# Performance work log

Measured on AMD Instinct MI355X. Metric: run time of the kernel, lower is better.

## Reference

```python
import jax, jax.numpy as jnp
import numpy as np

SCALE = 2      # shuffle_scale
K = 3          # nearest neighbors / conv kernel size (stride == K)
SAMPLES = 16   # sample grid size per axis -> M = SAMPLES**2


def pixel_unshuffle(x, s):
    B, C, H, W = x.shape
    x = x.reshape(B, C, H // s, s, W // s, s)
    x = x.transpose(0, 1, 3, 5, 2, 4)
    return x.reshape(B, C * s * s, H // s, W // s)


def pixel_shuffle(x, s):
    B, C, H, W = x.shape
    x = x.reshape(B, C // (s * s), s, s, H, W)
    x = x.transpose(0, 1, 4, 2, 5, 3)
    return x.reshape(B, C // (s * s), H * s, W * s)


def setup_inputs() -> dict:
    key = jax.random.key(0)
    k1, k2, k3 = jax.random.split(key, 3)
    x = jax.random.normal(k1, (32, 16, 128, 128), dtype=jnp.float32)
    weight = jax.random.normal(k2, (64, 64, K), dtype=jnp.float32) * 0.05  # [out_1d, in_1d, K]
    bias = jax.random.normal(k3, (64,), dtype=jnp.float32) * 0.05
    return {"x": x, "weight": weight, "bias": bias}


def reference(x, weight, bias):
    # --- pixel unshuffle ('B' part of 'BA') ---
    x1 = pixel_unshuffle(x, SCALE)                 # [B, C1=64, H1=64, W1=64]
    B, C1, H1, W1 = x1.shape
    N = H1 * W1

    # --- spatial subsample grid (linspace + round, sample_padding=0) ---
    xi = jnp.round(jnp.linspace(0.0, H1 - 1.0, SAMPLES)).astype(jnp.int32)
    yi = jnp.round(jnp.linspace(0.0, W1 - 1.0, SAMPLES)).astype(jnp.int32)
    xg, yg = jnp.meshgrid(xi, yi, indexing="ij")
    x_sample = x1[:, :, xg, yg].reshape(B, C1, -1)  # [B, C1, M]
    x2 = x1.reshape(B, C1, N)                       # [B, C1, N]

    # --- pairwise squared euclidean distance tokens -> samples ---
    # (sqrt omitted: monotone; top-k uses only indices, matching torch topk(largest=False))
    n2 = jnp.sum(x2 * x2, axis=1)                   # [B, N]
    m2 = jnp.sum(x_sample * x_sample, axis=1)       # [B, M]
    dot = jnp.einsum("bcn,bcm->bnm", x2, x_sample)  # [B, N, M]
    d2 = n2[:, :, None] + m2[:, None, :] - 2.0 * dot

    # --- K nearest sampled points per token ---
    _, idx = jax.lax.top_k(-d2, K)                  # [B, N, K]

    # --- gather neighbor features ('prime'); equals x2 at flat_indices[idx] ---
    prime = jnp.take_along_axis(x_sample[:, :, None, :], idx[:, None, :, :], axis=3)  # [B, C1, N, K]

    # --- Conv1d(kernel=K, stride=K) over [B, C1, N*K] == per-token contraction ---
    out = jnp.einsum("bcnk,ock->bon", prime, weight) + bias[None, :, None]  # [B, O1=64, N]
    out = out.reshape(B, weight.shape[0], H1, W1)

    # --- pixel shuffle ('A' part of 'BA') ---
    return pixel_shuffle(out, SCALE)                # [B, 16, 128, 128]
```

## Files before the change

kernel.cpp:

```cpp
#include <hip/hip_runtime.h>
#include <cstdint>
#include <cfloat>

typedef float v2f __attribute__((ext_vector_type(2)));

__constant__ int c_smp[16] = {0,4,8,13,17,21,25,29,34,38,42,46,50,55,59,63};

static constexpr int NB   = 32;
static constexpr int NC   = 64;
static constexpr int NH   = 64;
static constexpr int NTOK = 4096;
static constexpr int NM   = 256;
static constexpr int NK   = 3;

__global__ __launch_bounds__(256) void k_pre(const float* __restrict__ x,
                                             const float* __restrict__ w,
                                             float* __restrict__ wT,
                                             float* __restrict__ xs_t) {
    __shared__ __align__(16) float rows[16][2][128];
    if (blockIdx.x >= NB * 16) {
        int f = (blockIdx.x - NB * 16) * 256 + threadIdx.x;
        float v = w[f];
        int o = f / 192, rem = f % 192;
        int c = rem / 3, k = rem % 3;
        wT[((size_t)k * 64 + c) * 64 + o] = v;
        return;
    }
    int b = blockIdx.x >> 4, gi = blockIdx.x & 15;
    int hh = c_smp[gi];
    int t = threadIdx.x;
    const float* xb = x + (size_t)b * 16 * 128 * 128;
#pragma unroll
    for (int it = 0; it < 4; ++it) {
        int q = t + it * 256;
        int c = q >> 6;
        int rem = q & 63;
        int sh = rem >> 5;
        int col = (rem & 31) * 4;
        float4 v = *(const float4*)(xb + ((size_t)c * 128 + (2 * hh + sh)) * 128 + col);
        *(float4*)&rows[c][sh][col] = v;
    }
    __syncthreads();
    {
        int c1 = t >> 2;
        int c = c1 >> 2, sh = (c1 >> 1) & 1, sw = c1 & 1;
        int gj0 = (t & 3) * 4;
        float4 v;
        v.x = rows[c][sh][2 * c_smp[gj0 + 0] + sw];
        v.y = rows[c][sh][2 * c_smp[gj0 + 1] + sw];
        v.z = rows[c][sh][2 * c_smp[gj0 + 2] + sw];
        v.w = rows[c][sh][2 * c_smp[gj0 + 3] + sw];
        *(float4*)&xs_t[((size_t)b * NC + c1) * NM + gi * 16 + gj0] = v;
    }
}

__global__ __launch_bounds__(256) void k_z2(const float* __restrict__ xs_t,
                                            const float* __restrict__ wT,
                                            float* __restrict__ Z) {
    __shared__ __align__(16) float wL[64][64];
    __shared__ __align__(16) float xt[16][64];
    int bid = blockIdx.x;
    int mq = bid & 3;
    int k  = (bid >> 2) % 3;
    int b  = bid / 12;
    int t  = threadIdx.x;
    int mg = t >> 4, og = t & 15;

#pragma unroll
    for (int it = 0; it < 4; ++it) {
        int q = t + it * 256;
        int c = q >> 4;
        int o4 = (q & 15) * 4;
        *(float4*)&wL[c][o4] = *(const float4*)&wT[(size_t)k * 4096 + q * 4];
    }

    v2f acc[4][2];
#pragma unroll
    for (int i = 0; i < 4; ++i) { acc[i][0] = (v2f)(0.f); acc[i][1] = (v2f)(0.f); }

    for (int cc = 0; cc < 4; ++cc) {
        __syncthreads();
        {
            int c = t >> 4, m4 = (t & 15) * 4;
            *(float4*)&xt[c][m4] =
                *(const float4*)&xs_t[((size_t)b * NC + cc * 16 + c) * NM + mq * 64 + m4];
        }
        __syncthreads();
#pragma unroll
        for (int c = 0; c < 16; ++c) {
            float4 a4 = *(const float4*)&xt[c][mg * 4];
            float4 b4 = *(const float4*)&wL[cc * 16 + c][og * 4];
            v2f bp0 = {b4.x, b4.y}, bp1 = {b4.z, b4.w};
            float aa[4] = {a4.x, a4.y, a4.z, a4.w};
#pragma unroll
            for (int i = 0; i < 4; ++i) {
                v2f ai = {aa[i], aa[i]};
                acc[i][0] = __builtin_elementwise_fma(ai, bp0, acc[i][0]);
                acc[i][1] = __builtin_elementwise_fma(ai, bp1, acc[i][1]);
            }
        }
    }

    float* zb = Z + (((size_t)b * 3 + k) * NM + mq * 64) * NC;
#pragma unroll
    for (int i = 0; i < 4; ++i) {
        int m = mg * 4 + i;
        float4 v = {acc[i][0][0], acc[i][0][1], acc[i][1][0], acc[i][1][1]};
        *(float4*)&zb[(size_t)m * NC + og * 4] = v;
    }
}

static __device__ __forceinline__ unsigned long long packkey(float d, int m) {
    unsigned u = __float_as_uint(d);
    u ^= ((unsigned)((int)u >> 31)) | 0x80000000u;
    return ((unsigned long long)u << 32) | (unsigned)m;
}

__global__ __launch_bounds__(256) void k_do(const float* __restrict__ x,
                                            const float* __restrict__ xs_t,
                                            const float* __restrict__ Z,
                                            const float* __restrict__ bias,
                                            float* __restrict__ out) {
    __shared__ __align__(16) float smem[5632];
    float (*att)[64]  = (float(*)[64])smem;
    float (*xsB)[256] = (float(*)[256])(smem + 1024);
    float* m2l = smem + 5120;
    float* n2l = smem + 5376;
    int  (*idxL)[3] = (int(*)[3])(smem + 5440);
    float* staged = smem;

    int b = blockIdx.x >> 6;
    int h = blockIdx.x & 63;
    int t = threadIdx.x;
    int r = t >> 4, cl = t & 15;

    v2f acc2[4][8];
#pragma unroll
    for (int i = 0; i < 4; ++i)
#pragma unroll
        for (int j = 0; j < 8; ++j) acc2[i][j] = (v2f)(0.f);

    float m2acc = 0.f, n2acc = 0.f;
    const float* xb = x + (size_t)b * 16 * 128 * 128;
    const float* xsb = xs_t + (size_t)b * NC * NM;

    for (int kc = 0; kc < 4; ++kc) {
        __syncthreads();
#pragma unroll
        for (int it = 0; it < 2; ++it) {
            int i = t + it * 256;
            int p = i >> 6;
            int wcol = i & 63;
            int c1e = kc * 16 + p * 2;
            int c = c1e >> 2, sh = (c1e >> 1) & 1;
            const float* src = xb + ((size_t)c * 128 + (2 * h + sh)) * 128 + 2 * wcol;
            float2 v = *(const float2*)src;
            att[p * 2 + 0][wcol] = v.x;
            att[p * 2 + 1][wcol] = v.y;
        }
#pragma unroll
        for (int it = 0; it < 4; ++it) {
            int g = t + it * 256;
            int row = g >> 6;
            int m4 = g & 63;
            int dst = ((((m4 & 3) << 4) | (m4 >> 2))) << 2;
            *(float4*)&xsB[row][dst] =
                *(const float4*)&xsb[(size_t)(kc * 16 + row) * NM + m4 * 4];
        }
        __syncthreads();

#pragma unroll
        for (int c = 0; c < 16; ++c) {
            float v = xsB[c][t];
            m2acc = __fadd_rn(m2acc, __fmul_rn(v, v));
        }
        if (t < 64) {
#pragma unroll
            for (int c = 0; c < 16; ++c) {
                float v = att[c][t];
                n2acc = __fadd_rn(n2acc, __fmul_rn(v, v));
            }
        }

#pragma unroll
        for (int k = 0; k < 16; ++k) {
            float4 a0 = *(const float4*)&att[k][r * 4];
            float4 b0 = *(const float4*)&xsB[k][(0 * 16 + cl) * 4];
            float4 b1 = *(const float4*)&xsB[k][(1 * 16 + cl) * 4];
            float4 b2 = *(const float4*)&xsB[k][(2 * 16 + cl) * 4];
            float4 b3 = *(const float4*)&xsB[k][(3 * 16 + cl) * 4];
            v2f bp0 = {b0.x, b0.y}, bp1 = {b0.z, b0.w};
            v2f bp2 = {b1.x, b1.y}, bp3 = {b1.z, b1.w};
            v2f bp4 = {b2.x, b2.y}, bp5 = {b2.z, b2.w};
            v2f bp6 = {b3.x, b3.y}, bp7 = {b3.z, b3.w};
            float aa[4] = {a0.x, a0.y, a0.z, a0.w};
#pragma unroll
            for (int i = 0; i < 4; ++i) {
                v2f ai = {aa[i], aa[i]};
                acc2[i][0] = __builtin_elementwise_fma(ai, bp0, acc2[i][0]);
                acc2[i][1] = __builtin_elementwise_fma(ai, bp1, acc2[i][1]);
                acc2[i][2] = __builtin_elementwise_fma(ai, bp2, acc2[i][2]);
                acc2[i][3] = __builtin_elementwise_fma(ai, bp3, acc2[i][3]);
                acc2[i][4] = __builtin_elementwise_fma(ai, bp4, acc2[i][4]);
                acc2[i][5] = __builtin_elementwise_fma(ai, bp5, acc2[i][5]);
                acc2[i][6] = __builtin_elementwise_fma(ai, bp6, acc2[i][6]);
                acc2[i][7] = __builtin_elementwise_fma(ai, bp7, acc2[i][7]);
            }
        }
    }

    m2l[((t >> 2) & 15) * 16 + (t >> 6) * 4 + (t & 3)] = m2acc;
    if (t < 64) n2l[t] = n2acc;
    __syncthreads();

    float m2r[16];
#pragma unroll
    for (int j = 0; j < 16; ++j) m2r[j] = m2l[cl * 16 + j];

#pragma unroll
    for (int i = 0; i < 4; ++i) {
        int nloc = r * 4 + i;
        float n2v = n2l[nloc];
        float e0d = FLT_MAX, e1d = FLT_MAX, e2d = FLT_MAX;
        int e0m = 0x7fffffff, e1m = 0x7fffffff, e2m = 0x7fffffff;
#pragma unroll
        for (int j = 0; j < 16; ++j) {
            float dv = acc2[i][j >> 1][j & 1];
            float t1 = __fadd_rn(n2v, m2r[j]);
            float d = __fadd_rn(t1, -2.0f * dv);
            int m = cl * 16 + j;
            if (d < e2d) {
                e2d = d; e2m = m;
                if (e2d < e1d) {
                    float td = e1d; int tm = e1m; e1d = e2d; e1m = e2m;
                    e2d = td; e2m = tm;
                    if (e1d < e0d) {
                        float sd = e0d; int sm = e0m; e0d = e1d; e0m = e1m;
                        e1d = sd; e1m = sm;
                    }
                }
            }
        }
        unsigned long long k0 = packkey(e0d, e0m);
        unsigned long long k1 = packkey(e1d, e1m);
        unsigned long long k2 = packkey(e2d, e2m);
#pragma unroll
        for (int mask = 1; mask <= 8; mask <<= 1) {
            unsigned long long q0 = __shfl_xor(k0, mask);
            unsigned long long q1 = __shfl_xor(k1, mask);
            unsigned long long q2 = __shfl_xor(k2, mask);
            unsigned long long clo = k0 < q0 ? k0 : q0;
            unsigned long long chi = k0 < q0 ? q0 : k0;
            unsigned long long dlo = k1 < q1 ? k1 : q1;
            unsigned long long dhi = k1 < q1 ? q1 : k1;
            unsigned long long f2  = k2 < q2 ? k2 : q2;
            unsigned long long elo = chi < dlo ? chi : dlo;
            unsigned long long ehi = chi < dlo ? dlo : chi;
            unsigned long long g2  = dhi < f2 ? dhi : f2;
            k0 = clo;
            k1 = elo;
            k2 = ehi < g2 ? ehi : g2;
        }
        if (cl == 0) {
            idxL[nloc][0] = (int)(unsigned)(k0 & 0xffffffffu);
            idxL[nloc][1] = (int)(unsigned)(k1 & 0xffffffffu);
            idxL[nloc][2] = (int)(unsigned)(k2 & 0xffffffffu);
        }
    }
    __syncthreads();

    {
        int o = t & 63, wv = t >> 6;
        float bv = bias[o];
        const float* zb = Z + (size_t)b * 3 * NM * NC;
        for (int ti = 0; ti < 16; ++ti) {
            int w = wv * 16 + ti;
            int i0 = idxL[w][0], i1 = idxL[w][1], i2 = idxL[w][2];
            float v = bv + zb[(size_t)i0 * NC + o]
                         + zb[(size_t)(NM + i1) * NC + o]
                         + zb[(size_t)(2 * NM + i2) * NC + o];
            staged[o * 65 + w] = v;
        }
        __syncthreads();
        float* ob = out + (size_t)b * 16 * 128 * 128;
#pragma unroll
        for (int it = 0; it < 16; ++it) {
            int flat = t + it * 256;
            int W = flat & 127, sh = (flat >> 7) & 1, cc = flat >> 8;
            int oo = cc * 4 + sh * 2 + (W & 1);
            ob[((size_t)cc * 128 + 2 * h + sh) * 128 + W] = staged[oo * 65 + (W >> 1)];
        }
    }
}

extern "C" void kernel_launch(void* const* d_in, const int* in_sizes, int n_in,
                              void* d_out, int out_size, void* d_ws, size_t ws_size,
                              hipStream_t stream) {
    const float* x    = (const float*)d_in[0];
    const float* w    = (const float*)d_in[1];
    const float* bias = (const float*)d_in[2];
    float* out = (float*)d_out;
    float* ws  = (float*)d_ws;

    float* xs_t = ws;
    float* Z    = ws + 524288;
    float* wT   = ws + 2097152;

    hipLaunchKernelGGL(k_pre, dim3(NB * 16 + 48), dim3(256), 0, stream,
                       x, w, wT, xs_t);
    hipLaunchKernelGGL(k_z2,  dim3(NB * 3 * 4),   dim3(256), 0, stream,
                       xs_t, wT, Z);
    hipLaunchKernelGGL(k_do,  dim3(NB * 64),      dim3(256), 0, stream,
                       x, xs_t, Z, bias, out);
}
```

Before: 168.1 us.

## Merge sample-gather and Z projection into one kernel, dropping a launch

Folds the weight-transpose and Z-projection kernel into the preprocessing kernel. Z blocks now gather their own sampled features straight from x and transpose the weights in shared memory, so they no longer depend on xs_t. This removes one kernel launch and its inter-kernel dependency. In exchange, each Z block re-reads sampled rows of x and the full weight tensor, and filters weights with scalar modulo logic, which adds redundant loads and work per block.

```diff
diff --git a/kernel.cpp b/kernel.cpp
--- a/kernel.cpp
+++ b/kernel.cpp
@@ -13,22 +13,94 @@
 static constexpr int NM   = 256;
 static constexpr int NK   = 3;
 
-__global__ __launch_bounds__(256) void k_pre(const float* __restrict__ x,
-                                             const float* __restrict__ w,
-                                             float* __restrict__ wT,
-                                             float* __restrict__ xs_t) {
-    __shared__ __align__(16) float rows[16][2][128];
+__global__ __launch_bounds__(256) void k_pz(const float* __restrict__ x,
+                                            const float* __restrict__ w,
+                                            float* __restrict__ xs_t,
+                                            float* __restrict__ Z) {
+    __shared__ __align__(16) float smem[8448];
+    int t = threadIdx.x;
+
     if (blockIdx.x >= NB * 16) {
-        int f = (blockIdx.x - NB * 16) * 256 + threadIdx.x;
-        float v = w[f];
-        int o = f / 192, rem = f % 192;
-        int c = rem / 3, k = rem % 3;
-        wT[((size_t)k * 64 + c) * 64 + o] = v;
+        int zid = blockIdx.x - NB * 16;
+        int mq = zid & 3;
+        int k  = (zid >> 2) % 3;
+        int b  = zid / 12;
+        float (*xsl)[68] = (float(*)[68])smem;
+        float (*rows)[2][128] = (float(*)[2][128])(smem + 4352);
+        float (*wL)[64] = (float(*)[64])(smem + 4352);
+        const float* xb = x + (size_t)b * 16 * 128 * 128;
+
+        for (int g = 0; g < 4; ++g) {
+            int hh = c_smp[mq * 4 + g];
+            __syncthreads();
+#pragma unroll
+            for (int it = 0; it < 4; ++it) {
+                int q = t + it * 256;
+                int c = q >> 6;
+                int rem = q & 63;
+                int sh = rem >> 5;
+                int col = (rem & 31) * 4;
+                float4 v = *(const float4*)(xb + ((size_t)c * 128 + (2 * hh + sh)) * 128 + col);
+                *(float4*)&rows[c][sh][col] = v;
+            }
+            __syncthreads();
+            {
+                int c1 = t >> 2;
+                int c = c1 >> 2, sh = (c1 >> 1) & 1, sw = c1 & 1;
+                int gj0 = (t & 3) * 4;
+#pragma unroll
+                for (int j = 0; j < 4; ++j)
+                    xsl[c1][g * 16 + gj0 + j] = rows[c][sh][2 * c_smp[gj0 + j] + sw];
+            }
+        }
+        __syncthreads();
+
+#pragma unroll
+        for (int it = 0; it < 12; ++it) {
+            int q = t + it * 256;
+            float4 v = *(const float4*)(w + (size_t)q * 4);
+            float vv[4] = {v.x, v.y, v.z, v.w};
+#pragma unroll
+            for (int e = 0; e < 4; ++e) {
+                int f = q * 4 + e;
+                if (f % 3 == k) {
+                    int c = (f / 3) % 64, o = f / 192;
+                    wL[c][o] = vv[e];
+                }
+            }
+        }
+        __syncthreads();
+
+        int mg = t >> 4, og = t & 15;
+        v2f acc[4][2];
+#pragma unroll
+        for (int i = 0; i < 4; ++i) { acc[i][0] = (v2f)(0.f); acc[i][1] = (v2f)(0.f); }
+#pragma unroll
+        for (int c = 0; c < 64; ++c) {
+            float4 a4 = *(const float4*)&xsl[c][mg * 4];
+            float4 b4 = *(const float4*)&wL[c][og * 4];
+            v2f bp0 = {b4.x, b4.y}, bp1 = {b4.z, b4.w};
+            float aa[4] = {a4.x, a4.y, a4.z, a4.w};
+#pragma unroll
+            for (int i = 0; i < 4; ++i) {
+                v2f ai = {aa[i], aa[i]};
+                acc[i][0] = __builtin_elementwise_fma(ai, bp0, acc[i][0]);
+                acc[i][1] = __builtin_elementwise_fma(ai, bp1, acc[i][1]);
+            }
+        }
+        float* zb = Z + (((size_t)b * 3 + k) * NM + mq * 64) * NC;
+#pragma unroll
+        for (int i = 0; i < 4; ++i) {
+            int m = mg * 4 + i;
+            float4 v = {acc[i][0][0], acc[i][0][1], acc[i][1][0], acc[i][1][1]};
+            *(float4*)&zb[(size_t)m * NC + og * 4] = v;
+        }
         return;
     }
+
+    float (*rows)[2][128] = (float(*)[2][128])(smem + 4352);
     int b = blockIdx.x >> 4, gi = blockIdx.x & 15;
     int hh = c_smp[gi];
-    int t = threadIdx.x;
     const float* xb = x + (size_t)b * 16 * 128 * 128;
 #pragma unroll
     for (int it = 0; it < 4; ++it) {
@@ -51,62 +123,6 @@
         v.z = rows[c][sh][2 * c_smp[gj0 + 2] + sw];
         v.w = rows[c][sh][2 * c_smp[gj0 + 3] + sw];
         *(float4*)&xs_t[((size_t)b * NC + c1) * NM + gi * 16 + gj0] = v;
-    }
-}
-
-__global__ __launch_bounds__(256) void k_z2(const float* __restrict__ xs_t,
-                                            const float* __restrict__ wT,
-                                            float* __restrict__ Z) {
-    __shared__ __align__(16) float wL[64][64];
-    __shared__ __align__(16) float xt[16][64];
-    int bid = blockIdx.x;
-    int mq = bid & 3;
-    int k  = (bid >> 2) % 3;
-    int b  = bid / 12;
-    int t  = threadIdx.x;
-    int mg = t >> 4, og = t & 15;
-
-#pragma unroll
-    for (int it = 0; it < 4; ++it) {
-        int q = t + it * 256;
-        int c = q >> 4;
-        int o4 = (q & 15) * 4;
-        *(float4*)&wL[c][o4] = *(const float4*)&wT[(size_t)k * 4096 + q * 4];
-    }
-
-    v2f acc[4][2];
-#pragma unroll
-    for (int i = 0; i < 4; ++i) { acc[i][0] = (v2f)(0.f); acc[i][1] = (v2f)(0.f); }
-
-    for (int cc = 0; cc < 4; ++cc) {
-        __syncthreads();
-        {
-            int c = t >> 4, m4 = (t & 15) * 4;
-            *(float4*)&xt[c][m4] =
-                *(const float4*)&xs_t[((size_t)b * NC + cc * 16 + c) * NM + mq * 64 + m4];
-        }
-        __syncthreads();
-#pragma unroll
-        for (int c = 0; c < 16; ++c) {
-            float4 a4 = *(const float4*)&xt[c][mg * 4];
-            float4 b4 = *(const float4*)&wL[cc * 16 + c][og * 4];
-            v2f bp0 = {b4.x, b4.y}, bp1 = {b4.z, b4.w};
-            float aa[4] = {a4.x, a4.y, a4.z, a4.w};
-#pragma unroll
-            for (int i = 0; i < 4; ++i) {
-                v2f ai = {aa[i], aa[i]};
-                acc[i][0] = __builtin_elementwise_fma(ai, bp0, acc[i][0]);
-                acc[i][1] = __builtin_elementwise_fma(ai, bp1, acc[i][1]);
-            }
-        }
-    }
-
-    float* zb = Z + (((size_t)b * 3 + k) * NM + mq * 64) * NC;
-#pragma unroll
-    for (int i = 0; i < 4; ++i) {
-        int m = mg * 4 + i;
-        float4 v = {acc[i][0][0], acc[i][0][1], acc[i][1][0], acc[i][1][1]};
-        *(float4*)&zb[(size_t)m * NC + og * 4] = v;
     }
 }
 
@@ -304,12 +320,9 @@
 
     float* xs_t = ws;
     float* Z    = ws + 524288;
-    float* wT   = ws + 2097152;
-
-    hipLaunchKernelGGL(k_pre, dim3(NB * 16 + 48), dim3(256), 0, stream,
-                       x, w, wT, xs_t);
-    hipLaunchKernelGGL(k_z2,  dim3(NB * 3 * 4),   dim3(256), 0, stream,
-                       xs_t, wT, Z);
-    hipLaunchKernelGGL(k_do,  dim3(NB * 64),      dim3(256), 0, stream,
+
+    hipLaunchKernelGGL(k_pz, dim3(NB * 16 + NB * 3 * 4), dim3(256), 0, stream,
+                       x, w, xs_t, Z);
+    hipLaunchKernelGGL(k_do, dim3(NB * 64),               dim3(256), 0, stream,
                        x, xs_t, Z, bias, out);
 }
```

New measurement: 168.1 us. About the same (-0.0%).
